# Kernel optimization log

Hardware: AMD Instinct MI355X
Metric: run time of the kernel (lower is better)

Reference implementation:

```python
import jax, jax.numpy as jnp
import numpy as np

NEG_INF = -1e5  # module default neg_inf


def setup_inputs() -> dict:
    key = jax.random.key(0)
    k1, k2 = jax.random.split(key)
    B, T, V, U = 64, 1000, 512, 256
    log_posteriors = jax.random.normal(k1, (B, T, V), dtype=jnp.float32)
    lens = jnp.ones((B,), dtype=jnp.float32)
    phns = jax.random.randint(k2, (B, U), 0, V)
    phn_lens = jnp.ones((B,), dtype=jnp.float32)
    return {"log_posteriors": log_posteriors, "lens": lens, "phns": phns, "phn_lens": phn_lens}


def _forward_scores(log_posteriors, lens, phns, phn_lens):
    B, T, V = log_posteriors.shape
    U = phns.shape[1]
    lens_abs = jnp.round(lens * T).astype(jnp.int32)
    phn_lens_abs = jnp.round(phn_lens * U).astype(jnp.int32)

    # --- pi: all initial mass on first phoneme ---
    pi = jnp.full((B, U), NEG_INF, dtype=jnp.float32).at[:, 0].set(0.0)

    # --- transition log-probs: self-loop + advance-by-one, length-masked, row log_softmax ---
    base = jnp.eye(U, dtype=jnp.float32) + jnp.eye(U, k=1, dtype=jnp.float32)  # (U,U)
    m = jnp.arange(U)[None, :] < phn_lens_abs[:, None]  # (B,U) valid-phoneme mask
    m2 = m[:, :, None] & m[:, None, :]  # (B,U,U)
    masked = base[None, :, :] * m2.astype(jnp.float32)
    logits = jnp.where(masked == 1.0, 1.0, -jnp.inf)
    trans = jax.nn.log_softmax(logits, axis=2)
    # nan (all -inf rows) and -inf -> neg_inf, as in the torch module
    trans = jnp.where(jnp.isnan(trans) | jnp.isinf(trans), NEG_INF, trans)  # (B,U,U)

    # --- emissions rearranged to phoneme-sequence order: (B, U, T) as (T, B, U) scan seq ---
    mask_t = jnp.arange(T)[None, :] < lens_abs[:, None]  # (B,T)
    ep = jnp.where(mask_t[:, :, None], log_posteriors, NEG_INF)
    idx = jnp.broadcast_to(phns[:, None, :], (B, T, U))
    gathered = jnp.take_along_axis(ep, idx, axis=2)  # (B,T,U)
    emiss = jnp.where(m[:, None, :], gathered, NEG_INF)  # (B,T,U)
    emiss_seq = jnp.swapaxes(emiss, 0, 1)  # (T,B,U)

    # --- forward DP: alpha[t,i] = logsumexp_j(trans[j,i] + alpha[t-1,j]) + emiss[t,i] ---
    transT = jnp.swapaxes(trans, 1, 2)  # (B, to, from)
    alpha0 = pi + emiss_seq[0]  # (B,U), unmasked as in torch (masked entries ~2*neg_inf anyway)

    def step(alpha, e_t):
        x = jax.nn.logsumexp(transT + alpha[:, None, :], axis=2)  # batch_log_matvecmul
        alpha_new = jnp.where(m, x + e_t, NEG_INF)
        return alpha_new, None

    alphaT, _ = jax.lax.scan(step, alpha0, emiss_seq[1:])
    return jax.nn.logsumexp(alphaT, axis=1)  # (B,) log-likelihoods


def reference(log_posteriors, lens, phns, phn_lens):
    return _forward_scores(log_posteriors, lens, phns, phn_lens)
```

## Files before the change

kernel.cpp:

```cpp
#include <hip/hip_runtime.h>
#include <math.h>

constexpr int Bc = 64;
constexpr int Tc = 1000;
constexpr int Vc = 512;
constexpr int Uc = 256;
constexpr int CH = 50;
constexpr int NCH = Tc / CH;
constexpr int PW = 7;
constexpr int SLOTS = 4;

#define NEG_INF_F (-100000.0f)
#define LOG2E_F 1.44269504088896340736f
#define LN2_F 0.69314718055994530942f
#define DEAD_F (-1.0e9f)

__device__ __forceinline__ float fexp2(float x) {
#if __has_builtin(__builtin_amdgcn_exp2f)
    return __builtin_amdgcn_exp2f(x);
#else
    return __expf(x * LN2_F);
#endif
}
__device__ __forceinline__ float flog2(float x) {
#if __has_builtin(__builtin_amdgcn_logf)
    return __builtin_amdgcn_logf(x);
#else
    return __logf(x) * LOG2E_F;
#endif
}

__device__ __forceinline__ float l2add(float x, float y) {
    float m = fmaxf(x, y);
    float p = fexp2(-fabsf(x - y));
    return m + flog2(1.0f + p);
}

__device__ __forceinline__ void hmm_step(float rr[4], const float4 ev, float pen) {
    float nb0 = __shfl_up(rr[3], 1, 64) + pen;
    float e[4] = {ev.x, ev.y, ev.z, ev.w};
    float nb[4] = {nb0, rr[0], rr[1], rr[2]};
#pragma unroll
    for (int c = 0; c < 4; ++c) {
        float x = rr[c], y = nb[c];
        float m = fmaxf(x, y);
        float p = fexp2(-fabsf(x - y));
        rr[c] = m + flog2(1.0f + p) + e[c];
    }
}

__device__ __forceinline__ void dma16(const float* gsrc, float* lds, int lane) {
    typedef const __attribute__((address_space(1))) unsigned int* gp_t;
    typedef __attribute__((address_space(3))) unsigned int* lp_t;
    __builtin_amdgcn_global_load_lds((gp_t)(const void*)(gsrc + 4 * lane),
                                     (lp_t)(void*)lds, 16, 0, 0);
}

__global__ __launch_bounds__(512, 1) void fused_hmm_kernel(
    const float* __restrict__ lp, const float* __restrict__ lens,
    const int* __restrict__ phns, const float* __restrict__ phn_lens,
    float* __restrict__ out) {
    __shared__ float ebuf[2][CH][Uc];
    __shared__ float stage[PW][SLOTS][Vc];
    const int b = blockIdx.x;
    const int tid = threadIdx.x;
    const int wave = tid >> 6;
    const int lane = tid & 63;
    const int Tv = (int)rintf(lens[b] * (float)Tc);
    const int Uv = (int)rintf(phn_lens[b] * (float)Uc);
    const float* lpb = lp + (size_t)b * Tc * Vc;

    int col[4];
    float off[4];
    bool pv[4];
    float rr[4];
    const float pen = (lane == 0) ? DEAD_F : 0.0f;

    if (wave > 0) {
        int4 cc = *(const int4*)(phns + (size_t)b * Uc + 4 * lane);
        int c4[4] = {cc.x, cc.y, cc.z, cc.w};
#pragma unroll
        for (int c = 0; c < 4; ++c) {
            int v = c4[c];
            v = v < 0 ? 0 : (v > Vc - 1 ? Vc - 1 : v);
            col[c] = v;
            int i = 4 * lane + c;
            pv[c] = (i < Uv);
            off[c] = (i == Uv - 1) ? 0.0f : -1.0f;
        }
    }

    auto fill = [&](int k) {
        float* dst = &ebuf[k & 1][0][0];
        const int tb = k * CH;
        const int r0 = wave - 1;
        float* stw = &stage[wave - 1][0][0];
#pragma unroll
        for (int half = 0; half < 2; ++half) {
#pragma unroll
            for (int jj = 0; jj < SLOTS; ++jj) {
                int r = r0 + (half * SLOTS + jj) * PW;
                if (r < CH) {
                    const float* gsrc = lpb + (size_t)(tb + r) * Vc;
                    float* st = stw + jj * Vc;
                    dma16(gsrc, st, lane);
                    dma16(gsrc + 256, st + 256, lane);
                }
            }
            __builtin_amdgcn_s_waitcnt(0x0f70);
#pragma unroll
            for (int jj = 0; jj < SLOTS; ++jj) {
                int r = r0 + (half * SLOTS + jj) * PW;
                if (r < CH) {
                    const bool tv = (tb + r) < Tv;
                    const float* st = stw + jj * Vc;
                    float ev[4];
#pragma unroll
                    for (int c = 0; c < 4; ++c) {
                        float e = st[col[c]];
                        ev[c] = (pv[c] && tv) ? fmaf(e, LOG2E_F, off[c])
                                              : (NEG_INF_F * LOG2E_F + off[c]);
                    }
                    *(float4*)(dst + r * Uc + 4 * lane) =
                        make_float4(ev[0], ev[1], ev[2], ev[3]);
                }
            }
        }
    };

    auto consume = [&](int k) {
        const float4* base = (const float4*)&ebuf[k & 1][0][0] + lane;
        int r = 0;
        if (k == 0) {
            float4 e0 = base[0];
            float ea[4] = {e0.x, e0.y, e0.z, e0.w};
#pragma unroll
            for (int c = 0; c < 4; ++c)
                rr[c] = ((4 * lane + c == 0) ? 0.0f : DEAD_F) + ea[c];
            r = 1;
        }
        float4 q0, q1, q2, q3;
        if (r + 0 < CH) q0 = base[(r + 0) * 64];
        if (r + 1 < CH) q1 = base[(r + 1) * 64];
        if (r + 2 < CH) q2 = base[(r + 2) * 64];
        if (r + 3 < CH) q3 = base[(r + 3) * 64];
        while (r + 4 <= CH) {
            float4 e0 = q0, e1 = q1, e2 = q2, e3 = q3;
            if (r + 4 < CH) q0 = base[(r + 4) * 64];
            if (r + 5 < CH) q1 = base[(r + 5) * 64];
            if (r + 6 < CH) q2 = base[(r + 6) * 64];
            if (r + 7 < CH) q3 = base[(r + 7) * 64];
            hmm_step(rr, e0, pen);
            hmm_step(rr, e1, pen);
            hmm_step(rr, e2, pen);
            hmm_step(rr, e3, pen);
            r += 4;
        }
        if (r + 0 < CH) hmm_step(rr, q0, pen);
        if (r + 1 < CH) hmm_step(rr, q1, pen);
        if (r + 2 < CH) hmm_step(rr, q2, pen);
    };

    if (wave > 0) fill(0);
    __syncthreads();
    for (int k = 0; k < NCH; ++k) {
        if (wave > 0) {
            if (k + 1 < NCH) fill(k + 1);
        } else {
            consume(k);
        }
        __syncthreads();
    }

    if (wave == 0) {
        float a[4];
#pragma unroll
        for (int c = 0; c < 4; ++c)
            a[c] = rr[c] + ((4 * lane + c == Uv - 1) ? 0.0f : 1.0f);
        float r2 = l2add(l2add(a[0], a[1]), l2add(a[2], a[3]));
#pragma unroll
        for (int o = 32; o >= 1; o >>= 1) {
            float t = __shfl_xor(r2, o, 64);
            r2 = l2add(r2, t);
        }
        if (lane == 0) out[b] = r2 * LN2_F;
    }
}

extern "C" void kernel_launch(void* const* d_in, const int* in_sizes, int n_in,
                              void* d_out, int out_size, void* d_ws, size_t ws_size,
                              hipStream_t stream) {
    const float* lp = (const float*)d_in[0];
    const float* lens = (const float*)d_in[1];
    const int* phns = (const int*)d_in[2];
    const float* phn_lens = (const float*)d_in[3];
    float* out = (float*)d_out;
    (void)d_ws; (void)ws_size; (void)in_sizes; (void)n_in; (void)out_size;

    fused_hmm_kernel<<<Bc, 512, 0, stream>>>(lp, lens, phns, phn_lens, out);
}
```

Measured before the change: 273.8 us.

## Split fused HMM kernel into parallel gather kernel and lean scan kernel

```diff
diff --git a/kernel.cpp b/kernel.cpp
--- a/kernel.cpp
+++ b/kernel.cpp
@@ -10,6 +10,11 @@
 constexpr int PW = 7;
 constexpr int SLOTS = 4;
 
+constexpr int GW = 4;
+constexpr int GSL = 5;
+constexpr int GROWS = GW * GSL * 2;
+constexpr int GBLK = Tc / GROWS;
+
 #define NEG_INF_F (-100000.0f)
 #define LOG2E_F 1.44269504088896340736f
 #define LN2_F 0.69314718055994530942f
@@ -54,6 +59,146 @@
     typedef __attribute__((address_space(3))) unsigned int* lp_t;
     __builtin_amdgcn_global_load_lds((gp_t)(const void*)(gsrc + 4 * lane),
                                      (lp_t)(void*)lds, 16, 0, 0);
+}
+
+__global__ __launch_bounds__(256, 4) void gather_kernel(
+    const float* __restrict__ lp, const float* __restrict__ lens,
+    const int* __restrict__ phns, const float* __restrict__ phn_lens,
+    float* __restrict__ e2) {
+    __shared__ float stage[GW][GSL][Vc];
+    const int b = blockIdx.x;
+    const int t0 = blockIdx.y * GROWS;
+    const int tid = threadIdx.x;
+    const int wave = tid >> 6;
+    const int lane = tid & 63;
+    const int Tv = (int)rintf(lens[b] * (float)Tc);
+    const int Uv = (int)rintf(phn_lens[b] * (float)Uc);
+    const float* lpb = lp + (size_t)b * Tc * Vc;
+    float* e2b = e2 + ((size_t)b * Tc + t0) * Uc;
+
+    int col[4];
+    float off[4];
+    bool pv[4];
+    int4 cc = *(const int4*)(phns + (size_t)b * Uc + 4 * lane);
+    int c4[4] = {cc.x, cc.y, cc.z, cc.w};
+#pragma unroll
+    for (int c = 0; c < 4; ++c) {
+        int v = c4[c];
+        v = v < 0 ? 0 : (v > Vc - 1 ? Vc - 1 : v);
+        col[c] = v;
+        int i = 4 * lane + c;
+        pv[c] = (i < Uv);
+        off[c] = (i == Uv - 1) ? 0.0f : -1.0f;
+    }
+
+    float* stw = &stage[wave][0][0];
+#pragma unroll
+    for (int half = 0; half < 2; ++half) {
+#pragma unroll
+        for (int j = 0; j < GSL; ++j) {
+            int r = wave + (half * GSL + j) * GW;
+            const float* gsrc = lpb + (size_t)(t0 + r) * Vc;
+            float* st = stw + j * Vc;
+            dma16(gsrc, st, lane);
+            dma16(gsrc + 256, st + 256, lane);
+        }
+        __builtin_amdgcn_s_waitcnt(0x0f70);
+#pragma unroll
+        for (int j = 0; j < GSL; ++j) {
+            int r = wave + (half * GSL + j) * GW;
+            const bool tv = (t0 + r) < Tv;
+            const float* st = stw + j * Vc;
+            float ev[4];
+#pragma unroll
+            for (int c = 0; c < 4; ++c) {
+                float e = st[col[c]];
+                ev[c] = (pv[c] && tv) ? fmaf(e, LOG2E_F, off[c])
+                                      : (NEG_INF_F * LOG2E_F + off[c]);
+            }
+            *(float4*)(e2b + (size_t)r * Uc + 4 * lane) =
+                make_float4(ev[0], ev[1], ev[2], ev[3]);
+        }
+    }
+}
+
+__global__ __launch_bounds__(128, 1) void scan_kernel(
+    const float* __restrict__ e2, const float* __restrict__ phn_lens,
+    float* __restrict__ out) {
+    __shared__ float ebuf[2][CH][Uc];
+    const int b = blockIdx.x;
+    const int tid = threadIdx.x;
+    const int wave = tid >> 6;
+    const int lane = tid & 63;
+    const int Uv = (int)rintf(phn_lens[b] * (float)Uc);
+    const float* eb = e2 + (size_t)b * Tc * Uc;
+    float rr[4];
+    const float pen = (lane == 0) ? DEAD_F : 0.0f;
+
+    auto fill = [&](int k) {
+        const float* src = eb + (size_t)k * CH * Uc;
+        float* dst = &ebuf[k & 1][0][0];
+#pragma unroll 5
+        for (int r = 0; r < CH; ++r)
+            dma16(src + (size_t)r * Uc, dst + r * Uc, lane);
+    };
+
+    auto consume = [&](int k) {
+        const float4* base = (const float4*)&ebuf[k & 1][0][0] + lane;
+        int r = 0;
+        if (k == 0) {
+            float4 e0 = base[0];
+            float ea[4] = {e0.x, e0.y, e0.z, e0.w};
+#pragma unroll
+            for (int c = 0; c < 4; ++c)
+                rr[c] = ((4 * lane + c == 0) ? 0.0f : DEAD_F) + ea[c];
+            r = 1;
+        }
+        float4 q0, q1, q2, q3;
+        if (r + 0 < CH) q0 = base[(r + 0) * 64];
+        if (r + 1 < CH) q1 = base[(r + 1) * 64];
+        if (r + 2 < CH) q2 = base[(r + 2) * 64];
+        if (r + 3 < CH) q3 = base[(r + 3) * 64];
+        while (r + 4 <= CH) {
+            float4 e0 = q0, e1 = q1, e2v = q2, e3 = q3;
+            if (r + 4 < CH) q0 = base[(r + 4) * 64];
+            if (r + 5 < CH) q1 = base[(r + 5) * 64];
+            if (r + 6 < CH) q2 = base[(r + 6) * 64];
+            if (r + 7 < CH) q3 = base[(r + 7) * 64];
+            hmm_step(rr, e0, pen);
+            hmm_step(rr, e1, pen);
+            hmm_step(rr, e2v, pen);
+            hmm_step(rr, e3, pen);
+            r += 4;
+        }
+        if (r + 0 < CH) hmm_step(rr, q0, pen);
+        if (r + 1 < CH) hmm_step(rr, q1, pen);
+        if (r + 2 < CH) hmm_step(rr, q2, pen);
+    };
+
+    if (wave == 1) fill(0);
+    __syncthreads();
+    for (int k = 0; k < NCH; ++k) {
+        if (wave == 1) {
+            if (k + 1 < NCH) fill(k + 1);
+        } else {
+            consume(k);
+        }
+        __syncthreads();
+    }
+
+    if (wave == 0) {
+        float a[4];
+#pragma unroll
+        for (int c = 0; c < 4; ++c)
+            a[c] = rr[c] + ((4 * lane + c == Uv - 1) ? 0.0f : 1.0f);
+        float r2 = l2add(l2add(a[0], a[1]), l2add(a[2], a[3]));
+#pragma unroll
+        for (int o = 32; o >= 1; o >>= 1) {
+            float t = __shfl_xor(r2, o, 64);
+            r2 = l2add(r2, t);
+        }
+        if (lane == 0) out[b] = r2 * LN2_F;
+    }
 }
 
 __global__ __launch_bounds__(512, 1) void fused_hmm_kernel(
@@ -195,7 +340,15 @@
     const int* phns = (const int*)d_in[2];
     const float* phn_lens = (const float*)d_in[3];
     float* out = (float*)d_out;
-    (void)d_ws; (void)ws_size; (void)in_sizes; (void)n_in; (void)out_size;
-
-    fused_hmm_kernel<<<Bc, 512, 0, stream>>>(lp, lens, phns, phn_lens, out);
-}
+    (void)in_sizes; (void)n_in; (void)out_size;
+
+    const size_t need = (size_t)Bc * Tc * Uc * sizeof(float);
+    if (d_ws != nullptr && ws_size >= need) {
+        float* e2 = (float*)d_ws;
+        gather_kernel<<<dim3(Bc, GBLK), 256, 0, stream>>>(lp, lens, phns,
+                                                          phn_lens, e2);
+        scan_kernel<<<Bc, 128, 0, stream>>>(e2, phn_lens, out);
+    } else {
+        fused_hmm_kernel<<<Bc, 512, 0, stream>>>(lp, lens, phns, phn_lens, out);
+    }
+}
```

After: 321.9 us. 17.6% more time.
